# Optimization experiments

Measured on AMD Instinct MI355X. Metric: run time of the kernel, lower is better.

Reference implementation:

```python
import jax, jax.numpy as jnp
import numpy as np

LN_EPS = 1e-5


def _ssm_scan(x_ssm, A, Bm, C, reverse):
    # x_ssm: [B, L, d_inner]; A, Bm, C: [d_inner, d_state]
    Bb, L, di = x_ssm.shape
    ds = Bm.shape[1]

    def step(h, x_t):
        # h: [B, d_inner, d_state], x_t: [B, d_inner]
        h = jnp.clip(h * A[None] + x_t[:, :, None] * Bm[None], -10.0, 10.0)
        y = jnp.einsum('bid,id->bi', h, C)
        return h, y

    h0 = jnp.zeros((Bb, di, ds), x_ssm.dtype)
    _, ys = jax.lax.scan(step, h0, jnp.swapaxes(x_ssm, 0, 1), reverse=reverse)
    return jnp.swapaxes(ys, 0, 1)  # [B, L, d_inner], time-ordered


def setup_inputs() -> dict:
    key = jax.random.key(0)
    ks = jax.random.split(key, 6)
    B, L, D = 4, 2048, 1024
    d_state, expand = 16, 2
    d_inner = D * expand
    x = jax.random.normal(ks[0], (B, L, D), jnp.float32)
    # xavier-ish scaled params
    in_proj_w = jax.random.normal(ks[1], (d_inner * 2, D), jnp.float32) * np.float32(1.0 / np.sqrt(D))
    A_log = jax.random.normal(ks[2], (d_inner, d_state), jnp.float32)
    B_mat = jax.random.normal(ks[3], (d_inner, d_state), jnp.float32) * np.float32(1.0 / np.sqrt(d_state))
    C_mat = jnp.full((d_inner, d_state), 0.01, jnp.float32)
    out_proj_w = jax.random.normal(ks[4], (D, d_inner), jnp.float32) * np.float32(1.0 / np.sqrt(d_inner))
    ln_w = jnp.ones((D,), jnp.float32)
    ln_b = jnp.zeros((D,), jnp.float32)
    return {"x": x, "in_proj_w": in_proj_w, "A_log": A_log, "B_mat": B_mat,
            "C_mat": C_mat, "out_proj_w": out_proj_w, "ln_w": ln_w, "ln_b": ln_b}


def reference(x, in_proj_w, A_log, B_mat, C_mat, out_proj_w, ln_w, ln_b):
    # LayerNorm
    mu = jnp.mean(x, axis=-1, keepdims=True)
    var = jnp.mean((x - mu) ** 2, axis=-1, keepdims=True)
    xn = (x - mu) * jax.lax.rsqrt(var + LN_EPS) * ln_w + ln_b
    # in_proj (no bias), split into ssm stream and gate
    x_proj = jnp.einsum('bld,ed->ble', xn, in_proj_w)  # [B, L, 2*d_inner]
    x_ssm, gate = jnp.split(x_proj, 2, axis=-1)
    # A = -clamp(exp(A_log), -10, -0.01)  (saturates to 0.01, kept faithfully)
    A = -jnp.clip(jnp.exp(A_log), -10.0, -0.01)
    out_f = _ssm_scan(x_ssm, A, B_mat, C_mat, reverse=False)
    out_b = _ssm_scan(x_ssm, A, B_mat, C_mat, reverse=True)
    out = (out_f + out_b) * 0.5 * jax.nn.silu(gate)
    return jnp.einsum('bli,di->bld', out, out_proj_w)
```

## Files before the change

kernel.cpp:

```cpp
#include <hip/hip_runtime.h>

typedef __attribute__((ext_vector_type(8))) _Float16 f16x8;
typedef __attribute__((ext_vector_type(4))) float f32x4;

#define GLOBAL_AS __attribute__((address_space(1)))
#define LDS_AS __attribute__((address_space(3)))

static constexpr int Bb = 4, LL = 2048, DD = 1024, DI = 2048, DS = 16;
static constexpr int MROWS = Bb * LL;
static constexpr int N1 = 2 * DI;
static constexpr int K1 = DD;
static constexpr int N2 = DD;
static constexpr int K2 = DI;

__device__ __forceinline__ unsigned short f2h(float f) {
  _Float16 h = (_Float16)f;
  union { _Float16 h; unsigned short u; } c; c.h = h;
  return c.u;
}
__device__ __forceinline__ float h2f(unsigned short u) {
  union { unsigned short u; _Float16 h; } c; c.u = u;
  return (float)c.h;
}

__global__ __launch_bounds__(256) void ln_half_kernel(
    const float* __restrict__ x, const float* __restrict__ lnw,
    const float* __restrict__ lnb, unsigned short* __restrict__ A1) {
  const int r = blockIdx.x;
  const int tid = threadIdx.x;
  const float4 v = reinterpret_cast<const float4*>(x + (size_t)r * DD)[tid];
  float s = v.x + v.y + v.z + v.w;
#pragma unroll
  for (int off = 32; off >= 1; off >>= 1) s += __shfl_xor(s, off, 64);
  __shared__ float red[8];
  const int wid = tid >> 6;
  if ((tid & 63) == 0) red[wid] = s;
  __syncthreads();
  const float mu = (red[0] + red[1] + red[2] + red[3]) * (1.0f / DD);
  const float dx = v.x - mu, dy = v.y - mu, dz = v.z - mu, dw = v.w - mu;
  float ss = dx * dx + dy * dy + dz * dz + dw * dw;
#pragma unroll
  for (int off = 32; off >= 1; off >>= 1) ss += __shfl_xor(ss, off, 64);
  if ((tid & 63) == 0) red[4 + wid] = ss;
  __syncthreads();
  const float var = (red[4] + red[5] + red[6] + red[7]) * (1.0f / DD);
  const float rs = rsqrtf(var + 1e-5f);
  const float4 w4 = reinterpret_cast<const float4*>(lnw)[tid];
  const float4 b4 = reinterpret_cast<const float4*>(lnb)[tid];
  ushort4 h4;
  h4.x = f2h(dx * rs * w4.x + b4.x);
  h4.y = f2h(dy * rs * w4.y + b4.y);
  h4.z = f2h(dz * rs * w4.z + b4.z);
  h4.w = f2h(dw * rs * w4.w + b4.w);
  *reinterpret_cast<ushort4*>(&A1[(size_t)r * DD + tid * 4]) = h4;
}

__global__ __launch_bounds__(256) void f32_to_f16_kernel(
    const float* __restrict__ W, unsigned short* __restrict__ O) {
  const int gid = blockIdx.x * 256 + threadIdx.x;
  const float4 w = reinterpret_cast<const float4*>(W)[gid];
  ushort4 h4;
  h4.x = f2h(w.x); h4.y = f2h(w.y); h4.z = f2h(w.z); h4.w = f2h(w.w);
  reinterpret_cast<ushort4*>(O)[gid] = h4;
}

__global__ __launch_bounds__(512, 2) void gemm_bt_256(
    const unsigned short* __restrict__ A, const unsigned short* __restrict__ B,
    unsigned short* __restrict__ C, int M, int N, int K) {
  __shared__ unsigned short sm[4][2][256 * 32];
  const int tid = threadIdx.x;
  const int wid = tid >> 6;
  const int lane = tid & 63;
  const int wm = wid >> 2;
  const int wn = wid & 3;
  const int mt = M >> 8;
  const int cpx = gridDim.x >> 3;
  const int bid = blockIdx.x;
  const int sw = (bid & 7) * cpx + (bid >> 3);
  const int bm = sw % mt;
  const int bn = sw / mt;
  const size_t arow0 = (size_t)bm * 256;
  const size_t brow0 = (size_t)bn * 256;

  const unsigned short* gA[2];
  const unsigned short* gB[2];
#pragma unroll
  for (int j = 0; j < 2; ++j) {
    const int idx = j * 512 + tid;
    const int prow = idx >> 2;
    const int scol = ((idx & 3) ^ ((prow >> 1) & 3)) << 3;
    gA[j] = A + (arow0 + prow) * (size_t)K + scol;
    gB[j] = B + (brow0 + prow) * (size_t)K + scol;
  }
  auto stage = [&](int slot) {
#pragma unroll
    for (int j = 0; j < 2; ++j) {
      __builtin_amdgcn_global_load_lds((const GLOBAL_AS void*)gA[j],
          (LDS_AS void*)&sm[slot][0][(j * 512 + tid) * 8], 16, 0, 0);
      gA[j] += 32;
    }
#pragma unroll
    for (int j = 0; j < 2; ++j) {
      __builtin_amdgcn_global_load_lds((const GLOBAL_AS void*)gB[j],
          (LDS_AS void*)&sm[slot][1][(j * 512 + tid) * 8], 16, 0, 0);
      gB[j] += 32;
    }
  };

  const int q = lane >> 4;
  const int fr = lane & 15;
  const int swzk = ((q ^ ((fr >> 1) & 3)) << 3);

  int arows[8], brows[4];
#pragma unroll
  for (int mf = 0; mf < 8; ++mf) arows[mf] = ((wm << 7) + mf * 16 + fr) * 32;
#pragma unroll
  for (int nf = 0; nf < 4; ++nf) brows[nf] = ((wn << 6) + nf * 16 + fr) * 32;

  f32x4 acc[8][4] = {};

  const int NTK = K >> 5;
  stage(0);
  stage(1);

  for (int t = 0; t < NTK; ++t) {
    const int slot = t & 3;
    if (t + 2 < NTK) stage((t + 2) & 3);
    if (t + 2 < NTK)      asm volatile("s_waitcnt vmcnt(8)" ::: "memory");
    else if (t + 1 < NTK) asm volatile("s_waitcnt vmcnt(4)" ::: "memory");
    else                  asm volatile("s_waitcnt vmcnt(0)" ::: "memory");
    __builtin_amdgcn_s_barrier();
    __builtin_amdgcn_sched_barrier(0);
    f16x8 af[8], bf[4];
#pragma unroll
    for (int mf = 0; mf < 8; ++mf)
      af[mf] = *reinterpret_cast<const f16x8*>(&sm[slot][0][arows[mf] + swzk]);
#pragma unroll
    for (int nf = 0; nf < 4; ++nf)
      bf[nf] = *reinterpret_cast<const f16x8*>(&sm[slot][1][brows[nf] + swzk]);
#pragma unroll
    for (int mf = 0; mf < 8; ++mf)
#pragma unroll
      for (int nf = 0; nf < 4; ++nf)
        acc[mf][nf] = __builtin_amdgcn_mfma_f32_16x16x32_f16(
            af[mf], bf[nf], acc[mf][nf], 0, 0, 0);
  }

  const int fcol = lane & 15;
  const int frow4 = (lane >> 4) << 2;
#pragma unroll
  for (int mf = 0; mf < 8; ++mf)
#pragma unroll
    for (int nf = 0; nf < 4; ++nf) {
      const size_t row0 = arow0 + (wm << 7) + mf * 16 + frow4;
      const size_t col = brow0 + (wn << 6) + nf * 16 + fcol;
#pragma unroll
      for (int j = 0; j < 4; ++j)
        C[(row0 + j) * (size_t)N + col] = f2h(acc[mf][nf][j]);
    }
}

__global__ __launch_bounds__(512, 2) void gemm_bt_256n128(
    const unsigned short* __restrict__ A, const unsigned short* __restrict__ B,
    float* __restrict__ C, int M, int N, int K) {
  __shared__ unsigned short sm[2][24576];
  const int tid = threadIdx.x;
  const int wid = tid >> 6;
  const int lane = tid & 63;
  const int wm = wid >> 2;
  const int wn = wid & 3;
  const int mt = M >> 8;
  const int cpx = gridDim.x >> 3;
  const int bid = blockIdx.x;
  const int sw = (bid & 7) * cpx + (bid >> 3);
  const int bm = sw % mt;
  const int bn = sw / mt;
  const size_t arow0 = (size_t)bm * 256;
  const size_t brow0 = (size_t)bn * 128;

  const unsigned short* gA[4];
  const unsigned short* gB[2];
#pragma unroll
  for (int j = 0; j < 4; ++j) {
    const int idx = j * 512 + tid;
    const int prow = idx >> 3;
    const int scol = ((idx & 7) ^ (prow & 7)) << 3;
    gA[j] = A + (arow0 + prow) * (size_t)K + scol;
  }
#pragma unroll
  for (int j = 0; j < 2; ++j) {
    const int idx = j * 512 + tid;
    const int prow = idx >> 3;
    const int scol = ((idx & 7) ^ (prow & 7)) << 3;
    gB[j] = B + (brow0 + prow) * (size_t)K + scol;
  }
  auto stageA = [&](int buf) {
#pragma unroll
    for (int j = 0; j < 4; ++j) {
      __builtin_amdgcn_global_load_lds((const GLOBAL_AS void*)gA[j],
          (LDS_AS void*)&sm[buf][(j * 512 + (wid << 6)) * 8], 16, 0, 0);
      gA[j] += 64;
    }
  };
  auto stageB = [&](int buf) {
#pragma unroll
    for (int j = 0; j < 2; ++j) {
      __builtin_amdgcn_global_load_lds((const GLOBAL_AS void*)gB[j],
          (LDS_AS void*)&sm[buf][16384 + (j * 512 + (wid << 6)) * 8], 16, 0, 0);
      gB[j] += 64;
    }
  };

  const int q = lane >> 4;
  const int l7 = lane & 7;
  const int fr = lane & 15;
  int swz[2];
  swz[0] = (q << 3) ^ (l7 << 3);
  swz[1] = (32 + (q << 3)) ^ (l7 << 3);

  int arows[8], brows[2];
#pragma unroll
  for (int mf = 0; mf < 8; ++mf) arows[mf] = ((wm << 7) + mf * 16 + fr) * 64;
#pragma unroll
  for (int nf = 0; nf < 2; ++nf) brows[nf] = 16384 + ((wn << 5) + nf * 16 + fr) * 64;

  f32x4 acc[8][2] = {};

  const int NTK = K >> 6;
  stageA(0);
  stageB(0);
  __syncthreads();

  for (int t = 0; t < NTK; ++t) {
    const int cur = t & 1, nxt = cur ^ 1;
    if (t + 1 < NTK) { stageA(nxt); stageB(nxt); }
    f16x8 af[8][2], bf[2][2];
#pragma unroll
    for (int mf = 0; mf < 8; ++mf)
#pragma unroll
      for (int ks = 0; ks < 2; ++ks)
        af[mf][ks] = *reinterpret_cast<const f16x8*>(&sm[cur][arows[mf] + swz[ks]]);
#pragma unroll
    for (int nf = 0; nf < 2; ++nf)
#pragma unroll
      for (int ks = 0; ks < 2; ++ks)
        bf[nf][ks] = *reinterpret_cast<const f16x8*>(&sm[cur][brows[nf] + swz[ks]]);
#pragma unroll
    for (int ks = 0; ks < 2; ++ks)
#pragma unroll
      for (int mf = 0; mf < 8; ++mf)
#pragma unroll
        for (int nf = 0; nf < 2; ++nf)
          acc[mf][nf] = __builtin_amdgcn_mfma_f32_16x16x32_f16(
              af[mf][ks], bf[nf][ks], acc[mf][nf], 0, 0, 0);
    __syncthreads();
  }

  const int fcol = lane & 15;
  const int frow4 = (lane >> 4) << 2;
#pragma unroll
  for (int mf = 0; mf < 8; ++mf)
#pragma unroll
    for (int nf = 0; nf < 2; ++nf) {
      const size_t row0 = arow0 + (wm << 7) + mf * 16 + frow4;
      const size_t col = brow0 + (wn << 5) + nf * 16 + fcol;
#pragma unroll
      for (int j = 0; j < 4; ++j)
        C[(row0 + j) * (size_t)N + col] = acc[mf][nf][j];
    }
}

__global__ __launch_bounds__(256) void scan_kernel(
    const unsigned short* __restrict__ xp, const float* __restrict__ Bm,
    const float* __restrict__ Cm, unsigned short* __restrict__ oss) {
  constexpr int T = 32, KH = 8;
  const int blk = blockIdx.x;
  const int igrp = blk & 7;
  const int c = (blk >> 3) & 63;
  const int b = blk >> 9;
  const int tid = threadIdx.x;
  const int i = igrp * 256 + tid;
  float d = 0.f;
  {
    const float4* bp = reinterpret_cast<const float4*>(Bm + (size_t)i * DS);
    const float4* cp = reinterpret_cast<const float4*>(Cm + (size_t)i * DS);
#pragma unroll
    for (int qv = 0; qv < 4; ++qv) {
      const float4 bv = bp[qv], cv = cp[qv];
      d += bv.x * cv.x + bv.y * cv.y + bv.z * cv.z + bv.w * cv.w;
    }
  }
  const float dh = 0.5f * d;
  const int t0 = c * T;
  const size_t rowbase = (size_t)b * LL;
  float yf[T];
  float g = 0.f;
  {
    const int hstart = (t0 >= KH) ? t0 - KH : 0;
    for (int t = hstart; t < t0; ++t)
      g = fmaf(0.01f, g, h2f(xp[(rowbase + t) * (size_t)N1 + i]));
#pragma unroll
    for (int j = 0; j < T; ++j) {
      g = fmaf(0.01f, g, h2f(xp[(rowbase + t0 + j) * (size_t)N1 + i]));
      yf[j] = g;
    }
  }
  g = 0.f;
  {
    const int tend = (t0 + T - 1 + KH <= LL - 1) ? (t0 + T - 1 + KH) : (LL - 1);
    for (int t = tend; t >= t0 + T; --t)
      g = fmaf(0.01f, g, h2f(xp[(rowbase + t) * (size_t)N1 + i]));
#pragma unroll
    for (int j = T - 1; j >= 0; --j) {
      const size_t row = rowbase + t0 + j;
      g = fmaf(0.01f, g, h2f(xp[row * (size_t)N1 + i]));
      const float gt = h2f(xp[row * (size_t)N1 + DI + i]);
      const float sg = gt / (1.f + expf(-gt));
      const float o = (yf[j] + g) * dh * sg;
      oss[row * (size_t)DI + i] = f2h(o);
    }
  }
}

extern "C" void kernel_launch(void* const* d_in, const int* in_sizes, int n_in,
                              void* d_out, int out_size, void* d_ws, size_t ws_size,
                              hipStream_t stream) {
  (void)in_sizes; (void)n_in; (void)out_size; (void)ws_size;
  const float* x          = (const float*)d_in[0];
  const float* in_proj_w  = (const float*)d_in[1];
  const float* B_mat      = (const float*)d_in[3];
  const float* C_mat      = (const float*)d_in[4];
  const float* out_proj_w = (const float*)d_in[5];
  const float* ln_w       = (const float*)d_in[6];
  const float* ln_b       = (const float*)d_in[7];
  float* out = (float*)d_out;

  char* ws = (char*)d_ws;
  unsigned short* A1  = (unsigned short*)ws; ws += (size_t)MROWS * K1 * 2;
  unsigned short* B1  = (unsigned short*)ws; ws += (size_t)N1 * K1 * 2;
  unsigned short* B2  = (unsigned short*)ws; ws += (size_t)N2 * K2 * 2;
  unsigned short* OSS = (unsigned short*)ws; ws += (size_t)MROWS * DI * 2;
  unsigned short* XP  = (unsigned short*)ws; ws += (size_t)MROWS * N1 * 2;

  f32_to_f16_kernel<<<dim3((N1 * K1 / 4) / 256), dim3(256), 0, stream>>>(in_proj_w, B1);
  f32_to_f16_kernel<<<dim3((N2 * K2 / 4) / 256), dim3(256), 0, stream>>>(out_proj_w, B2);
  ln_half_kernel<<<dim3(MROWS), dim3(256), 0, stream>>>(x, ln_w, ln_b, A1);
  gemm_bt_256<<<dim3((MROWS / 256) * (N1 / 256)), dim3(512), 0, stream>>>(A1, B1, XP, MROWS, N1, K1);
  scan_kernel<<<dim3(2048), dim3(256), 0, stream>>>(XP, B_mat, C_mat, OSS);
  gemm_bt_256n128<<<dim3((MROWS / 256) * (N2 / 128)), dim3(512), 0, stream>>>(OSS, B2, out, MROWS, N2, K2);
}
```

Baseline: 187.8 us.

## Split GEMM k-steps into ping-pong MFMA halves and vectorize scan loads

Both GEMMs now interleave LDS fragment reads, async global-to-LDS prefetch of A and B, and two half-batches of MFMAs, with barriers and s_setprio around each batch. The aim is to hide load latency behind matrix work. The second GEMM moves from a 2-stage BK=64 pipeline to a 4-slot BK=32 ring using the same swizzle as the first GEMM. The scan kernel now handles two channels per thread, using 32-bit loads and stores and half the blocks, to cut memory instruction count. The cost is more barriers per k-step and more registers per scan thread.

```diff
diff --git a/kernel.cpp b/kernel.cpp
--- a/kernel.cpp
+++ b/kernel.cpp
@@ -92,13 +92,15 @@
     gA[j] = A + (arow0 + prow) * (size_t)K + scol;
     gB[j] = B + (brow0 + prow) * (size_t)K + scol;
   }
-  auto stage = [&](int slot) {
+  auto stageA = [&](int slot) {
 #pragma unroll
     for (int j = 0; j < 2; ++j) {
       __builtin_amdgcn_global_load_lds((const GLOBAL_AS void*)gA[j],
           (LDS_AS void*)&sm[slot][0][(j * 512 + tid) * 8], 16, 0, 0);
       gA[j] += 32;
     }
+  };
+  auto stageB = [&](int slot) {
 #pragma unroll
     for (int j = 0; j < 2; ++j) {
       __builtin_amdgcn_global_load_lds((const GLOBAL_AS void*)gB[j],
@@ -120,30 +122,52 @@
   f32x4 acc[8][4] = {};
 
   const int NTK = K >> 5;
-  stage(0);
-  stage(1);
+  stageA(0); stageB(0);
+  stageA(1); stageB(1);
+  asm volatile("s_waitcnt vmcnt(4)" ::: "memory");
+  __builtin_amdgcn_s_barrier();
 
   for (int t = 0; t < NTK; ++t) {
     const int slot = t & 3;
-    if (t + 2 < NTK) stage((t + 2) & 3);
-    if (t + 2 < NTK)      asm volatile("s_waitcnt vmcnt(8)" ::: "memory");
-    else if (t + 1 < NTK) asm volatile("s_waitcnt vmcnt(4)" ::: "memory");
-    else                  asm volatile("s_waitcnt vmcnt(0)" ::: "memory");
-    __builtin_amdgcn_s_barrier();
-    __builtin_amdgcn_sched_barrier(0);
+    const bool pf = (t + 2 < NTK);
     f16x8 af[8], bf[4];
 #pragma unroll
-    for (int mf = 0; mf < 8; ++mf)
+    for (int mf = 0; mf < 4; ++mf)
       af[mf] = *reinterpret_cast<const f16x8*>(&sm[slot][0][arows[mf] + swzk]);
 #pragma unroll
     for (int nf = 0; nf < 4; ++nf)
       bf[nf] = *reinterpret_cast<const f16x8*>(&sm[slot][1][brows[nf] + swzk]);
-#pragma unroll
-    for (int mf = 0; mf < 8; ++mf)
+    if (pf) stageA((t + 2) & 3);
+    __builtin_amdgcn_s_barrier();
+    asm volatile("s_waitcnt lgkmcnt(0)" ::: "memory");
+    __builtin_amdgcn_sched_barrier(0);
+    __builtin_amdgcn_s_setprio(1);
+#pragma unroll
+    for (int mf = 0; mf < 4; ++mf)
 #pragma unroll
       for (int nf = 0; nf < 4; ++nf)
         acc[mf][nf] = __builtin_amdgcn_mfma_f32_16x16x32_f16(
             af[mf], bf[nf], acc[mf][nf], 0, 0, 0);
+    __builtin_amdgcn_s_setprio(0);
+    __builtin_amdgcn_s_barrier();
+#pragma unroll
+    for (int mf = 0; mf < 4; ++mf)
+      af[4 + mf] = *reinterpret_cast<const f16x8*>(&sm[slot][0][arows[4 + mf] + swzk]);
+    if (pf) stageB((t + 2) & 3);
+    __builtin_amdgcn_s_barrier();
+    asm volatile("s_waitcnt lgkmcnt(0)" ::: "memory");
+    __builtin_amdgcn_sched_barrier(0);
+    __builtin_amdgcn_s_setprio(1);
+#pragma unroll
+    for (int mf = 0; mf < 4; ++mf)
+#pragma unroll
+      for (int nf = 0; nf < 4; ++nf)
+        acc[4 + mf][nf] = __builtin_amdgcn_mfma_f32_16x16x32_f16(
+            af[4 + mf], bf[nf], acc[4 + mf][nf], 0, 0, 0);
+    __builtin_amdgcn_s_setprio(0);
+    if (pf)                   asm volatile("s_waitcnt vmcnt(4)" ::: "memory");
+    else if (t + 1 < NTK)     asm volatile("s_waitcnt vmcnt(0)" ::: "memory");
+    __builtin_amdgcn_s_barrier();
   }
 
   const int fcol = lane & 15;
@@ -163,7 +187,7 @@
 __global__ __launch_bounds__(512, 2) void gemm_bt_256n128(
     const unsigned short* __restrict__ A, const unsigned short* __restrict__ B,
     float* __restrict__ C, int M, int N, int K) {
-  __shared__ unsigned short sm[2][24576];
+  __shared__ unsigned short sm[4][12288];
   const int tid = threadIdx.x;
   const int wid = tid >> 6;
   const int lane = tid & 63;
@@ -178,82 +202,93 @@
   const size_t arow0 = (size_t)bm * 256;
   const size_t brow0 = (size_t)bn * 128;
 
-  const unsigned short* gA[4];
-  const unsigned short* gB[2];
-#pragma unroll
-  for (int j = 0; j < 4; ++j) {
-    const int idx = j * 512 + tid;
-    const int prow = idx >> 3;
-    const int scol = ((idx & 7) ^ (prow & 7)) << 3;
-    gA[j] = A + (arow0 + prow) * (size_t)K + scol;
-  }
+  const unsigned short* gA[2];
+  const unsigned short* gB0;
 #pragma unroll
   for (int j = 0; j < 2; ++j) {
     const int idx = j * 512 + tid;
-    const int prow = idx >> 3;
-    const int scol = ((idx & 7) ^ (prow & 7)) << 3;
-    gB[j] = B + (brow0 + prow) * (size_t)K + scol;
-  }
-  auto stageA = [&](int buf) {
-#pragma unroll
-    for (int j = 0; j < 4; ++j) {
+    const int prow = idx >> 2;
+    const int scol = ((idx & 3) ^ ((prow >> 1) & 3)) << 3;
+    gA[j] = A + (arow0 + prow) * (size_t)K + scol;
+  }
+  {
+    const int prow = tid >> 2;
+    const int scol = ((tid & 3) ^ ((prow >> 1) & 3)) << 3;
+    gB0 = B + (brow0 + prow) * (size_t)K + scol;
+  }
+  auto stageA = [&](int slot) {
+#pragma unroll
+    for (int j = 0; j < 2; ++j) {
       __builtin_amdgcn_global_load_lds((const GLOBAL_AS void*)gA[j],
-          (LDS_AS void*)&sm[buf][(j * 512 + (wid << 6)) * 8], 16, 0, 0);
-      gA[j] += 64;
+          (LDS_AS void*)&sm[slot][(j * 512 + tid) * 8], 16, 0, 0);
+      gA[j] += 32;
     }
   };
-  auto stageB = [&](int buf) {
-#pragma unroll
-    for (int j = 0; j < 2; ++j) {
-      __builtin_amdgcn_global_load_lds((const GLOBAL_AS void*)gB[j],
-          (LDS_AS void*)&sm[buf][16384 + (j * 512 + (wid << 6)) * 8], 16, 0, 0);
-      gB[j] += 64;
-    }
+  auto stageB = [&](int slot) {
+    __builtin_amdgcn_global_load_lds((const GLOBAL_AS void*)gB0,
+        (LDS_AS void*)&sm[slot][8192 + tid * 8], 16, 0, 0);
+    gB0 += 32;
   };
 
   const int q = lane >> 4;
-  const int l7 = lane & 7;
   const int fr = lane & 15;
-  int swz[2];
-  swz[0] = (q << 3) ^ (l7 << 3);
-  swz[1] = (32 + (q << 3)) ^ (l7 << 3);
+  const int swzk = ((q ^ ((fr >> 1) & 3)) << 3);
 
   int arows[8], brows[2];
 #pragma unroll
-  for (int mf = 0; mf < 8; ++mf) arows[mf] = ((wm << 7) + mf * 16 + fr) * 64;
-#pragma unroll
-  for (int nf = 0; nf < 2; ++nf) brows[nf] = 16384 + ((wn << 5) + nf * 16 + fr) * 64;
+  for (int mf = 0; mf < 8; ++mf) arows[mf] = ((wm << 7) + mf * 16 + fr) * 32;
+#pragma unroll
+  for (int nf = 0; nf < 2; ++nf) brows[nf] = 8192 + ((wn << 5) + nf * 16 + fr) * 32;
 
   f32x4 acc[8][2] = {};
 
-  const int NTK = K >> 6;
-  stageA(0);
-  stageB(0);
-  __syncthreads();
+  const int NTK = K >> 5;
+  stageA(0); stageB(0);
+  stageA(1); stageB(1);
+  asm volatile("s_waitcnt vmcnt(3)" ::: "memory");
+  __builtin_amdgcn_s_barrier();
 
   for (int t = 0; t < NTK; ++t) {
-    const int cur = t & 1, nxt = cur ^ 1;
-    if (t + 1 < NTK) { stageA(nxt); stageB(nxt); }
-    f16x8 af[8][2], bf[2][2];
-#pragma unroll
-    for (int mf = 0; mf < 8; ++mf)
-#pragma unroll
-      for (int ks = 0; ks < 2; ++ks)
-        af[mf][ks] = *reinterpret_cast<const f16x8*>(&sm[cur][arows[mf] + swz[ks]]);
+    const int slot = t & 3;
+    const bool pf = (t + 2 < NTK);
+    f16x8 af[8], bf[2];
+#pragma unroll
+    for (int mf = 0; mf < 4; ++mf)
+      af[mf] = *reinterpret_cast<const f16x8*>(&sm[slot][arows[mf] + swzk]);
 #pragma unroll
     for (int nf = 0; nf < 2; ++nf)
-#pragma unroll
-      for (int ks = 0; ks < 2; ++ks)
-        bf[nf][ks] = *reinterpret_cast<const f16x8*>(&sm[cur][brows[nf] + swz[ks]]);
-#pragma unroll
-    for (int ks = 0; ks < 2; ++ks)
-#pragma unroll
-      for (int mf = 0; mf < 8; ++mf)
-#pragma unroll
-        for (int nf = 0; nf < 2; ++nf)
-          acc[mf][nf] = __builtin_amdgcn_mfma_f32_16x16x32_f16(
-              af[mf][ks], bf[nf][ks], acc[mf][nf], 0, 0, 0);
-    __syncthreads();
+      bf[nf] = *reinterpret_cast<const f16x8*>(&sm[slot][brows[nf] + swzk]);
+    if (pf) stageA((t + 2) & 3);
+    __builtin_amdgcn_s_barrier();
+    asm volatile("s_waitcnt lgkmcnt(0)" ::: "memory");
+    __builtin_amdgcn_sched_barrier(0);
+    __builtin_amdgcn_s_setprio(1);
+#pragma unroll
+    for (int mf = 0; mf < 4; ++mf)
+#pragma unroll
+      for (int nf = 0; nf < 2; ++nf)
+        acc[mf][nf] = __builtin_amdgcn_mfma_f32_16x16x32_f16(
+            af[mf], bf[nf], acc[mf][nf], 0, 0, 0);
+    __builtin_amdgcn_s_setprio(0);
+    __builtin_amdgcn_s_barrier();
+#pragma unroll
+    for (int mf = 0; mf < 4; ++mf)
+      af[4 + mf] = *reinterpret_cast<const f16x8*>(&sm[slot][arows[4 + mf] + swzk]);
+    if (pf) stageB((t + 2) & 3);
+    __builtin_amdgcn_s_barrier();
+    asm volatile("s_waitcnt lgkmcnt(0)" ::: "memory");
+    __builtin_amdgcn_sched_barrier(0);
+    __builtin_amdgcn_s_setprio(1);
+#pragma unroll
+    for (int mf = 0; mf < 4; ++mf)
+#pragma unroll
+      for (int nf = 0; nf < 2; ++nf)
+        acc[4 + mf][nf] = __builtin_amdgcn_mfma_f32_16x16x32_f16(
+            af[4 + mf], bf[nf], acc[4 + mf][nf], 0, 0, 0);
+    __builtin_amdgcn_s_setprio(0);
+    if (pf)                   asm volatile("s_waitcnt vmcnt(3)" ::: "memory");
+    else if (t + 1 < NTK)     asm volatile("s_waitcnt vmcnt(0)" ::: "memory");
+    __builtin_amdgcn_s_barrier();
   }
 
   const int fcol = lane & 15;
@@ -275,49 +310,72 @@
     const float* __restrict__ Cm, unsigned short* __restrict__ oss) {
   constexpr int T = 32, KH = 8;
   const int blk = blockIdx.x;
-  const int igrp = blk & 7;
-  const int c = (blk >> 3) & 63;
-  const int b = blk >> 9;
+  const int igrp = blk & 3;
+  const int c = (blk >> 2) & 63;
+  const int b = blk >> 8;
   const int tid = threadIdx.x;
-  const int i = igrp * 256 + tid;
-  float d = 0.f;
-  {
-    const float4* bp = reinterpret_cast<const float4*>(Bm + (size_t)i * DS);
-    const float4* cp = reinterpret_cast<const float4*>(Cm + (size_t)i * DS);
+  const int i0 = igrp * 512 + tid * 2;
+  float d0 = 0.f, d1 = 0.f;
+#pragma unroll
+  for (int ch = 0; ch < 2; ++ch) {
+    const float4* bp = reinterpret_cast<const float4*>(Bm + (size_t)(i0 + ch) * DS);
+    const float4* cp = reinterpret_cast<const float4*>(Cm + (size_t)(i0 + ch) * DS);
+    float d = 0.f;
 #pragma unroll
     for (int qv = 0; qv < 4; ++qv) {
       const float4 bv = bp[qv], cv = cp[qv];
       d += bv.x * cv.x + bv.y * cv.y + bv.z * cv.z + bv.w * cv.w;
     }
-  }
-  const float dh = 0.5f * d;
+    if (ch == 0) d0 = d; else d1 = d;
+  }
+  const float dh0 = 0.5f * d0, dh1 = 0.5f * d1;
   const int t0 = c * T;
   const size_t rowbase = (size_t)b * LL;
-  float yf[T];
-  float g = 0.f;
+  float yf0[T], yf1[T];
+  float g0 = 0.f, g1 = 0.f;
   {
     const int hstart = (t0 >= KH) ? t0 - KH : 0;
-    for (int t = hstart; t < t0; ++t)
-      g = fmaf(0.01f, g, h2f(xp[(rowbase + t) * (size_t)N1 + i]));
+    for (int t = hstart; t < t0; ++t) {
+      const unsigned int u = *reinterpret_cast<const unsigned int*>(
+          xp + (rowbase + t) * (size_t)N1 + i0);
+      g0 = fmaf(0.01f, g0, h2f((unsigned short)(u & 0xffff)));
+      g1 = fmaf(0.01f, g1, h2f((unsigned short)(u >> 16)));
+    }
 #pragma unroll
     for (int j = 0; j < T; ++j) {
-      g = fmaf(0.01f, g, h2f(xp[(rowbase + t0 + j) * (size_t)N1 + i]));
-      yf[j] = g;
-    }
-  }
-  g = 0.f;
+      const unsigned int u = *reinterpret_cast<const unsigned int*>(
+          xp + (rowbase + t0 + j) * (size_t)N1 + i0);
+      g0 = fmaf(0.01f, g0, h2f((unsigned short)(u & 0xffff)));
+      g1 = fmaf(0.01f, g1, h2f((unsigned short)(u >> 16)));
+      yf0[j] = g0; yf1[j] = g1;
+    }
+  }
+  g0 = 0.f; g1 = 0.f;
   {
     const int tend = (t0 + T - 1 + KH <= LL - 1) ? (t0 + T - 1 + KH) : (LL - 1);
-    for (int t = tend; t >= t0 + T; --t)
-      g = fmaf(0.01f, g, h2f(xp[(rowbase + t) * (size_t)N1 + i]));
+    for (int t = tend; t >= t0 + T; --t) {
+      const unsigned int u = *reinterpret_cast<const unsigned int*>(
+          xp + (rowbase + t) * (size_t)N1 + i0);
+      g0 = fmaf(0.01f, g0, h2f((unsigned short)(u & 0xffff)));
+      g1 = fmaf(0.01f, g1, h2f((unsigned short)(u >> 16)));
+    }
 #pragma unroll
     for (int j = T - 1; j >= 0; --j) {
       const size_t row = rowbase + t0 + j;
-      g = fmaf(0.01f, g, h2f(xp[row * (size_t)N1 + i]));
-      const float gt = h2f(xp[row * (size_t)N1 + DI + i]);
-      const float sg = gt / (1.f + expf(-gt));
-      const float o = (yf[j] + g) * dh * sg;
-      oss[row * (size_t)DI + i] = f2h(o);
+      const unsigned int u = *reinterpret_cast<const unsigned int*>(
+          xp + row * (size_t)N1 + i0);
+      g0 = fmaf(0.01f, g0, h2f((unsigned short)(u & 0xffff)));
+      g1 = fmaf(0.01f, g1, h2f((unsigned short)(u >> 16)));
+      const unsigned int ug = *reinterpret_cast<const unsigned int*>(
+          xp + row * (size_t)N1 + DI + i0);
+      const float gt0 = h2f((unsigned short)(ug & 0xffff));
+      const float gt1 = h2f((unsigned short)(ug >> 16));
+      const float sg0 = gt0 / (1.f + expf(-gt0));
+      const float sg1 = gt1 / (1.f + expf(-gt1));
+      const float o0 = (yf0[j] + g0) * dh0 * sg0;
+      const float o1 = (yf1[j] + g1) * dh1 * sg1;
+      const unsigned int up = (unsigned int)f2h(o0) | ((unsigned int)f2h(o1) << 16);
+      *reinterpret_cast<unsigned int*>(oss + row * (size_t)DI + i0) = up;
     }
   }
 }
@@ -346,6 +404,6 @@
   f32_to_f16_kernel<<<dim3((N2 * K2 / 4) / 256), dim3(256), 0, stream>>>(out_proj_w, B2);
   ln_half_kernel<<<dim3(MROWS), dim3(256), 0, stream>>>(x, ln_w, ln_b, A1);
   gemm_bt_256<<<dim3((MROWS / 256) * (N1 / 256)), dim3(512), 0, stream>>>(A1, B1, XP, MROWS, N1, K1);
-  scan_kernel<<<dim3(2048), dim3(256), 0, stream>>>(XP, B_mat, C_mat, OSS);
+  scan_kernel<<<dim3(1024), dim3(256), 0, stream>>>(XP, B_mat, C_mat, OSS);
   gemm_bt_256n128<<<dim3((MROWS / 256) * (N2 / 128)), dim3(512), 0, stream>>>(OSS, B2, out, MROWS, N2, K2);
 }
```

Result: slower. 195.7 us (+4.2%).
